# Kernel tuning notes

Hardware: AMD Instinct MI355X
Metric: run time of the kernel (lower is better)

Reference implementation:

```python
import jax, jax.numpy as jnp
import numpy as np

TOPK = 4
TEMP = 1.0
BN_EPS = 1e-5


def setup_inputs() -> dict:
    key = jax.random.key(0)
    ks = jax.random.split(key, 5)
    B, H, W = 8, 256, 256
    return {
        "img": jax.random.uniform(ks[0], (B, 3, H, W), dtype=jnp.float32),
        "feat": jax.random.normal(ks[1], (B, 64, H, W), dtype=jnp.float32),
        "w_bneck": jax.random.normal(ks[2], (16, 64), dtype=jnp.float32) * 0.1,
        "b_bneck": jax.random.normal(ks[3], (16,), dtype=jnp.float32) * 0.1,
        "gamma": jnp.ones((16,), dtype=jnp.float32),
        "beta": jnp.zeros((16,), dtype=jnp.float32),
        "w_mask": jax.random.normal(ks[4], (256, 16), dtype=jnp.float32) * 0.1,
        "num_colors": 64,
    }


def reference(img, feat, w_bneck, b_bneck, gamma, beta, w_mask, num_colors):
    B, _, H, W = img.shape
    # bottleneck: 1x1 conv + BatchNorm (training stats) + ReLU
    x = jnp.einsum('bchw,oc->bohw', feat, w_bneck) + b_bneck[None, :, None, None]
    mu = x.mean(axis=(0, 2, 3))
    var = x.var(axis=(0, 2, 3))
    x = (x - mu[None, :, None, None]) * jax.lax.rsqrt(var + BN_EPS)[None, :, None, None]
    x = jax.nn.relu(x * gamma[None, :, None, None] + beta[None, :, None, None])
    # color_mask: bias-free 1x1 conv -> [B, 256, H, W]
    m = jnp.einsum('bchw,oc->bohw', x, w_mask)
    # agg == 'mean': [B, 256//num_colors, num_colors, H, W].mean(1)
    m = m.reshape(B, -1, num_colors, H, W).mean(axis=1)  # [B, nc, H, W]
    # per-pixel topk over color channel + softmax + scatter mask
    k = min(TOPK, num_colors)
    m_l = jnp.transpose(m, (0, 2, 3, 1))          # [B, H, W, nc]
    vals, idx = jax.lax.top_k(m_l, k)             # [B, H, W, k]
    sm = jax.nn.softmax(vals / TEMP, axis=-1)
    bi = jnp.arange(B)[:, None, None, None]
    hi = jnp.arange(H)[None, :, None, None]
    wi = jnp.arange(W)[None, None, :, None]
    m_scat = jnp.zeros_like(m_l).at[bi, hi, wi, idx].set(sm)
    m = jnp.transpose(m_scat, (0, 3, 1, 2))       # [B, nc, H, W]
    # weighted color palette: [B, 3, nc, 1, 1]
    num = jnp.einsum('bchw,bnhw->bcn', img, m)
    den = m.sum(axis=(2, 3))                      # [B, nc]
    color_palette = (num / (den[:, None, :] + 1e-8))[:, :, :, None, None]
    # train-mode reconstruction
    transformed_img = jnp.einsum('bnhw,bcn->bchw', m, color_palette[:, :, :, 0, 0])
    return (transformed_img, m, color_palette)
```

## Files before the change

kernel.cpp:

```cpp
#include <hip/hip_runtime.h>

typedef long long ll;

#define PPI   65536
#define NPIX  524288
#define NCH   64
#define NB    16
#define NC    64
#define BN_EPS 1e-5

__global__ __launch_bounds__(256) void k_stats(const float* __restrict__ feat,
                                               const float* __restrict__ wb,
                                               const float* __restrict__ bb,
                                               double* __restrict__ gsum,
                                               double* __restrict__ gsq)
{
    const int P = 4;
    int tid = threadIdx.x;
    int b   = blockIdx.x >> 6;
    int p0  = (blockIdx.x & 63) * 1024 + tid;
    const float* fb = feat + (ll)b * NCH * PPI + p0;

    float acc[NB][P];
#pragma unroll
    for (int o = 0; o < NB; ++o)
#pragma unroll
        for (int j = 0; j < P; ++j) acc[o][j] = 0.f;

#pragma unroll 4
    for (int c = 0; c < NCH; ++c) {
        float f[P];
#pragma unroll
        for (int j = 0; j < P; ++j) f[j] = fb[(ll)c * PPI + j * 256];
#pragma unroll
        for (int o = 0; o < NB; ++o) {
            float wv = wb[o * NCH + c];
#pragma unroll
            for (int j = 0; j < P; ++j) acc[o][j] = fmaf(f[j], wv, acc[o][j]);
        }
    }

    __shared__ float wsum[4][NB];
    __shared__ float wsq[4][NB];
    int wave = tid >> 6, lane = tid & 63;
#pragma unroll
    for (int o = 0; o < NB; ++o) {
        float bo = bb[o];
        float s = 0.f, q = 0.f;
#pragma unroll
        for (int j = 0; j < P; ++j) { float x = acc[o][j] + bo; s += x; q = fmaf(x, x, q); }
        for (int off = 32; off > 0; off >>= 1) {
            s += __shfl_down(s, off);
            q += __shfl_down(q, off);
        }
        if (lane == 0) { wsum[wave][o] = s; wsq[wave][o] = q; }
    }
    __syncthreads();
    if (tid < NB) {
        double s = (double)wsum[0][tid] + wsum[1][tid] + wsum[2][tid] + wsum[3][tid];
        double q = (double)wsq[0][tid] + wsq[1][tid] + wsq[2][tid] + wsq[3][tid];
        atomicAdd(&gsum[tid], s);
        atomicAdd(&gsq[tid], q);
    }
}

__global__ void k_finalize(const double* __restrict__ gsum,
                           const double* __restrict__ gsq,
                           const float* __restrict__ gamma,
                           const float* __restrict__ beta,
                           const float* __restrict__ wm,
                           float* __restrict__ scl,
                           float* __restrict__ shf,
                           float* __restrict__ weff)
{
    int t = threadIdx.x;
    if (t < NB) {
        double mu  = gsum[t] / (double)NPIX;
        double var = gsq[t] / (double)NPIX - mu * mu;
        double sc  = (double)gamma[t] / sqrt(var + BN_EPS);
        scl[t] = (float)sc;
        shf[t] = (float)((double)beta[t] - mu * sc);
    }
    if (t < NC) {
#pragma unroll
        for (int o = 0; o < NB; ++o) {
            float v = 0.25f * (wm[(0 * 64 + t) * NB + o] + wm[(1 * 64 + t) * NB + o] +
                               wm[(2 * 64 + t) * NB + o] + wm[(3 * 64 + t) * NB + o]);
            weff[t * NB + o] = v;
        }
    }
}

__global__ __launch_bounds__(256) void k_main(const float* __restrict__ feat,
                                              const float* __restrict__ img,
                                              const float* __restrict__ wb,
                                              const float* __restrict__ bb,
                                              const float* __restrict__ scl,
                                              const float* __restrict__ shf,
                                              const float* __restrict__ weff,
                                              float* __restrict__ m_out,
                                              unsigned* __restrict__ idx_out,
                                              float* __restrict__ sm_out,
                                              float* __restrict__ den_g,
                                              float* __restrict__ num_g)
{
    const int P = 2;
    __shared__ float den_loc[NC];
    __shared__ float num_loc[3 * NC];
    int tid = threadIdx.x;
    if (tid < NC) den_loc[tid] = 0.f;
    if (tid < 3 * NC) num_loc[tid] = 0.f;
    __syncthreads();

    int b  = blockIdx.x >> 7;
    int p0 = (blockIdx.x & 127) * 512 + tid;
    const float* fb = feat + (ll)b * NCH * PPI + p0;

    float acc[NB][P];
#pragma unroll
    for (int o = 0; o < NB; ++o)
#pragma unroll
        for (int j = 0; j < P; ++j) acc[o][j] = 0.f;

#pragma unroll 4
    for (int c = 0; c < NCH; ++c) {
        float f[P];
#pragma unroll
        for (int j = 0; j < P; ++j) f[j] = fb[(ll)c * PPI + j * 256];
#pragma unroll
        for (int o = 0; o < NB; ++o) {
            float wv = wb[o * NCH + c];
#pragma unroll
            for (int j = 0; j < P; ++j) acc[o][j] = fmaf(f[j], wv, acc[o][j]);
        }
    }

#pragma unroll
    for (int o = 0; o < NB; ++o) {
        float sc = scl[o];
        float sh = fmaf(bb[o], sc, shf[o]);
#pragma unroll
        for (int j = 0; j < P; ++j) acc[o][j] = fmaxf(0.f, fmaf(acc[o][j], sc, sh));
    }

    float tv[P][4];
    int   ti[P][4];
#pragma unroll
    for (int j = 0; j < P; ++j)
#pragma unroll
        for (int k = 0; k < 4; ++k) { tv[j][k] = -3.4e38f; ti[j][k] = 0; }

    for (int n = 0; n < NC; ++n) {
        float v[P];
#pragma unroll
        for (int j = 0; j < P; ++j) v[j] = 0.f;
#pragma unroll
        for (int o = 0; o < NB; ++o) {
            float wv = weff[n * NB + o];
#pragma unroll
            for (int j = 0; j < P; ++j) v[j] = fmaf(acc[o][j], wv, v[j]);
        }
#pragma unroll
        for (int j = 0; j < P; ++j) {
            float vv = v[j];
            if (vv > tv[j][3]) {
                if (vv > tv[j][0]) {
                    tv[j][3] = tv[j][2]; ti[j][3] = ti[j][2];
                    tv[j][2] = tv[j][1]; ti[j][2] = ti[j][1];
                    tv[j][1] = tv[j][0]; ti[j][1] = ti[j][0];
                    tv[j][0] = vv;       ti[j][0] = n;
                } else if (vv > tv[j][1]) {
                    tv[j][3] = tv[j][2]; ti[j][3] = ti[j][2];
                    tv[j][2] = tv[j][1]; ti[j][2] = ti[j][1];
                    tv[j][1] = vv;       ti[j][1] = n;
                } else if (vv > tv[j][2]) {
                    tv[j][3] = tv[j][2]; ti[j][3] = ti[j][2];
                    tv[j][2] = vv;       ti[j][2] = n;
                } else {
                    tv[j][3] = vv;       ti[j][3] = n;
                }
            }
        }
    }

    float sm[P][4];
#pragma unroll
    for (int j = 0; j < P; ++j) {
        float m0 = tv[j][0];
        float e0 = 1.0f;
        float e1 = expf(tv[j][1] - m0);
        float e2 = expf(tv[j][2] - m0);
        float e3 = expf(tv[j][3] - m0);
        float Z  = e0 + e1 + e2 + e3;
        sm[j][0] = e0 / Z; sm[j][1] = e1 / Z; sm[j][2] = e2 / Z; sm[j][3] = e3 / Z;
    }

#pragma unroll 1
    for (int n = 0; n < NC; ++n) {
#pragma unroll
        for (int j = 0; j < P; ++j) {
            float val = 0.f;
            val = (n == ti[j][0]) ? sm[j][0] : val;
            val = (n == ti[j][1]) ? sm[j][1] : val;
            val = (n == ti[j][2]) ? sm[j][2] : val;
            val = (n == ti[j][3]) ? sm[j][3] : val;
            m_out[((ll)b * NC + n) * PPI + p0 + j * 256] = val;
        }
    }

#pragma unroll
    for (int j = 0; j < P; ++j) {
        int p = p0 + j * 256;
        ll gp = (ll)b * PPI + p;
        idx_out[gp] = (unsigned)ti[j][0] | ((unsigned)ti[j][1] << 8) |
                      ((unsigned)ti[j][2] << 16) | ((unsigned)ti[j][3] << 24);
        sm_out[gp]             = sm[j][0];
        sm_out[(ll)NPIX + gp]  = sm[j][1];
        sm_out[2ll * NPIX + gp] = sm[j][2];
        sm_out[3ll * NPIX + gp] = sm[j][3];
        float i0 = img[((ll)b * 3 + 0) * PPI + p];
        float i1 = img[((ll)b * 3 + 1) * PPI + p];
        float i2 = img[((ll)b * 3 + 2) * PPI + p];
#pragma unroll
        for (int k = 0; k < 4; ++k) {
            float s = sm[j][k];
            int   n = ti[j][k];
            atomicAdd(&den_loc[n], s);
            atomicAdd(&num_loc[n], s * i0);
            atomicAdd(&num_loc[NC + n], s * i1);
            atomicAdd(&num_loc[2 * NC + n], s * i2);
        }
    }
    __syncthreads();
    if (tid < NC)     atomicAdd(&den_g[b * NC + tid], den_loc[tid]);
    if (tid < 3 * NC) atomicAdd(&num_g[(ll)b * 3 * NC + tid], num_loc[tid]);
}

__global__ void k_palette(const float* __restrict__ den_g,
                          const float* __restrict__ num_g,
                          float* __restrict__ pal_out)
{
    int t = blockIdx.x * blockDim.x + threadIdx.x;
    if (t >= 8 * NC) return;
    int b = t >> 6, n = t & 63;
    float d = den_g[t] + 1e-8f;
#pragma unroll
    for (int c = 0; c < 3; ++c)
        pal_out[((ll)b * 3 + c) * NC + n] = num_g[((ll)b * 3 + c) * NC + n] / d;
}

__global__ __launch_bounds__(256) void k_recon(const unsigned* __restrict__ idx_in,
                                               const float* __restrict__ sm_in,
                                               const float* __restrict__ pal,
                                               float* __restrict__ tout)
{
    const int P = 4;
    __shared__ float lpal[3 * NC];
    int tid = threadIdx.x;
    int b   = blockIdx.x >> 6;
    int p0  = (blockIdx.x & 63) * 1024 + tid;
    if (tid < 3 * NC) lpal[tid] = pal[(ll)b * 3 * NC + tid];
    __syncthreads();

#pragma unroll
    for (int j = 0; j < P; ++j) {
        int p = p0 + j * 256;
        ll gp = (ll)b * PPI + p;
        unsigned pk = idx_in[gp];
        int t0 = pk & 255, t1 = (pk >> 8) & 255, t2 = (pk >> 16) & 255, t3 = pk >> 24;
        float s0 = sm_in[gp];
        float s1 = sm_in[(ll)NPIX + gp];
        float s2 = sm_in[2ll * NPIX + gp];
        float s3 = sm_in[3ll * NPIX + gp];
#pragma unroll
        for (int c = 0; c < 3; ++c) {
            float v = s0 * lpal[c * NC + t0] + s1 * lpal[c * NC + t1] +
                      s2 * lpal[c * NC + t2] + s3 * lpal[c * NC + t3];
            tout[((ll)b * 3 + c) * PPI + p] = v;
        }
    }
}

extern "C" void kernel_launch(void* const* d_in, const int* in_sizes, int n_in,
                              void* d_out, int out_size, void* d_ws, size_t ws_size,
                              hipStream_t stream)
{
    const float* img   = (const float*)d_in[0];
    const float* feat  = (const float*)d_in[1];
    const float* wb    = (const float*)d_in[2];
    const float* bb    = (const float*)d_in[3];
    const float* gamma = (const float*)d_in[4];
    const float* beta  = (const float*)d_in[5];
    const float* wm    = (const float*)d_in[6];

    char* ws = (char*)d_ws;
    double*   gsum  = (double*)(ws + 0);
    double*   gsq   = (double*)(ws + 128);
    float*    den_g = (float*)(ws + 256);
    float*    num_g = (float*)(ws + 2304);
    float*    weff  = (float*)(ws + 8448);
    float*    scl   = (float*)(ws + 12544);
    float*    shf   = (float*)(ws + 12608);
    unsigned* idx4  = (unsigned*)(ws + 12672);
    float*    smarr = (float*)(ws + 12672 + 4ll * NPIX);

    float* t_out   = (float*)d_out;
    float* m_out   = t_out + 3ll * NPIX;
    float* pal_out = m_out + 64ll * NPIX;

    hipMemsetAsync(ws, 0, 8448, stream);

    k_stats<<<NPIX / 1024, 256, 0, stream>>>(feat, wb, bb, gsum, gsq);
    k_finalize<<<1, 64, 0, stream>>>(gsum, gsq, gamma, beta, wm, scl, shf, weff);
    k_main<<<NPIX / 512, 256, 0, stream>>>(feat, img, wb, bb, scl, shf, weff,
                                           m_out, idx4, smarr, den_g, num_g);
    k_palette<<<2, 256, 0, stream>>>(den_g, num_g, pal_out);
    k_recon<<<NPIX / 1024, 256, 0, stream>>>(idx4, smarr, pal_out, t_out);
}
```

Before: 361.9 us.

## Store bottleneck conv output once, fold finalize/palette kernels, vectorize with float4

The feature 1x1 conv is now computed once. Its pre-BN output is stashed in the last 16 channel planes of the m output buffer, so the second full read of the 64-channel feature tensor goes away. BN finalize and weight averaging move into the mask kernel, and palette division moves into recon, cutting two launches. All kernels now process 4 contiguous pixels per thread with float4 loads and stores. Top-k becomes a branchless select network, and shared-memory atomics are split per wave. The scratch reuse of m_out relies on every mask block reading its stashed planes before any block overwrites them, and a block's own channel 48-63 writes to its own pixels happen after its read.

```diff
diff --git a/kernel.cpp b/kernel.cpp
--- a/kernel.cpp
+++ b/kernel.cpp
@@ -9,275 +9,254 @@
 #define NC    64
 #define BN_EPS 1e-5
 
-__global__ __launch_bounds__(256) void k_stats(const float* __restrict__ feat,
-                                               const float* __restrict__ wb,
-                                               const float* __restrict__ bb,
-                                               double* __restrict__ gsum,
-                                               double* __restrict__ gsq)
-{
-    const int P = 4;
-    int tid = threadIdx.x;
-    int b   = blockIdx.x >> 6;
-    int p0  = (blockIdx.x & 63) * 1024 + tid;
+__global__ __launch_bounds__(256) void k_conv(const float* __restrict__ feat,
+                                              const float* __restrict__ wb,
+                                              double* __restrict__ gsum,
+                                              double* __restrict__ gsq,
+                                              float* __restrict__ xout)
+{
+    const int tid = threadIdx.x;
+    const int wave = tid >> 6, lane = tid & 63;
+    const int b   = blockIdx.x >> 6;
+    const int p0  = ((blockIdx.x & 63) << 10) + (tid << 2);
     const float* fb = feat + (ll)b * NCH * PPI + p0;
 
-    float acc[NB][P];
-#pragma unroll
-    for (int o = 0; o < NB; ++o)
-#pragma unroll
-        for (int j = 0; j < P; ++j) acc[o][j] = 0.f;
+    float4 acc[NB];
+#pragma unroll
+    for (int o = 0; o < NB; ++o) acc[o] = make_float4(0.f, 0.f, 0.f, 0.f);
 
 #pragma unroll 4
     for (int c = 0; c < NCH; ++c) {
-        float f[P];
-#pragma unroll
-        for (int j = 0; j < P; ++j) f[j] = fb[(ll)c * PPI + j * 256];
+        float4 f = *reinterpret_cast<const float4*>(fb + (ll)c * PPI);
 #pragma unroll
         for (int o = 0; o < NB; ++o) {
             float wv = wb[o * NCH + c];
-#pragma unroll
-            for (int j = 0; j < P; ++j) acc[o][j] = fmaf(f[j], wv, acc[o][j]);
-        }
-    }
-
-    __shared__ float wsum[4][NB];
-    __shared__ float wsq[4][NB];
-    int wave = tid >> 6, lane = tid & 63;
+            acc[o].x = fmaf(f.x, wv, acc[o].x);
+            acc[o].y = fmaf(f.y, wv, acc[o].y);
+            acc[o].z = fmaf(f.z, wv, acc[o].z);
+            acc[o].w = fmaf(f.w, wv, acc[o].w);
+        }
+    }
+
+#pragma unroll
+    for (int o = 0; o < NB; ++o)
+        *reinterpret_cast<float4*>(xout + ((ll)(b * NC + 48 + o)) * PPI + p0) = acc[o];
+
+    __shared__ float red_s[4][NB], red_q[4][NB];
 #pragma unroll
     for (int o = 0; o < NB; ++o) {
-        float bo = bb[o];
-        float s = 0.f, q = 0.f;
-#pragma unroll
-        for (int j = 0; j < P; ++j) { float x = acc[o][j] + bo; s += x; q = fmaf(x, x, q); }
+        float s = (acc[o].x + acc[o].y) + (acc[o].z + acc[o].w);
+        float q = fmaf(acc[o].x, acc[o].x, acc[o].y * acc[o].y) +
+                  fmaf(acc[o].z, acc[o].z, acc[o].w * acc[o].w);
+#pragma unroll
         for (int off = 32; off > 0; off >>= 1) {
             s += __shfl_down(s, off);
             q += __shfl_down(q, off);
         }
-        if (lane == 0) { wsum[wave][o] = s; wsq[wave][o] = q; }
+        if (lane == 0) { red_s[wave][o] = s; red_q[wave][o] = q; }
     }
     __syncthreads();
     if (tid < NB) {
-        double s = (double)wsum[0][tid] + wsum[1][tid] + wsum[2][tid] + wsum[3][tid];
-        double q = (double)wsq[0][tid] + wsq[1][tid] + wsq[2][tid] + wsq[3][tid];
-        atomicAdd(&gsum[tid], s);
-        atomicAdd(&gsq[tid], q);
-    }
-}
-
-__global__ void k_finalize(const double* __restrict__ gsum,
-                           const double* __restrict__ gsq,
-                           const float* __restrict__ gamma,
-                           const float* __restrict__ beta,
-                           const float* __restrict__ wm,
-                           float* __restrict__ scl,
-                           float* __restrict__ shf,
-                           float* __restrict__ weff)
-{
-    int t = threadIdx.x;
-    if (t < NB) {
-        double mu  = gsum[t] / (double)NPIX;
-        double var = gsq[t] / (double)NPIX - mu * mu;
-        double sc  = (double)gamma[t] / sqrt(var + BN_EPS);
-        scl[t] = (float)sc;
-        shf[t] = (float)((double)beta[t] - mu * sc);
-    }
-    if (t < NC) {
+        atomicAdd(&gsum[tid], (double)red_s[0][tid] + red_s[1][tid] + red_s[2][tid] + red_s[3][tid]);
+        atomicAdd(&gsq[tid],  (double)red_q[0][tid] + red_q[1][tid] + red_q[2][tid] + red_q[3][tid]);
+    }
+}
+
+__global__ __launch_bounds__(256) void k_mask(const float* __restrict__ img,
+                                              const float* __restrict__ gamma,
+                                              const float* __restrict__ beta,
+                                              const float* __restrict__ wm,
+                                              const double* __restrict__ gsum,
+                                              const double* __restrict__ gsq,
+                                              float* __restrict__ den_g,
+                                              float* __restrict__ num_g,
+                                              float* m_out,
+                                              unsigned* __restrict__ idx_out,
+                                              float* __restrict__ sm_out)
+{
+    __shared__ float weff_l[NC][NB];
+    __shared__ float den_loc[4][NC];
+    __shared__ float num_loc[4][3 * NC];
+    __shared__ float scl_l[NB], shf_l[NB];
+
+    const int tid = threadIdx.x;
+    const int wave = tid >> 6;
+    const int b   = blockIdx.x >> 6;
+    const int p0  = ((blockIdx.x & 63) << 10) + (tid << 2);
+
+    for (int i = tid; i < NC * NB; i += 256) {
+        int n = i >> 4, o = i & 15;
+        weff_l[n][o] = 0.25f * (wm[n * NB + o] + wm[(64 + n) * NB + o] +
+                                wm[(128 + n) * NB + o] + wm[(192 + n) * NB + o]);
+    }
+    for (int i = tid; i < 4 * NC; i += 256) den_loc[i >> 6][i & 63] = 0.f;
+    for (int i = tid; i < 4 * 3 * NC; i += 256) num_loc[i / (3 * NC)][i % (3 * NC)] = 0.f;
+    if (tid < NB) {
+        double mu  = gsum[tid] * (1.0 / NPIX);
+        double var = gsq[tid] * (1.0 / NPIX) - mu * mu;
+        double sc  = (double)gamma[tid] / sqrt(var + BN_EPS);
+        scl_l[tid] = (float)sc;
+        shf_l[tid] = (float)((double)beta[tid] - mu * sc);
+    }
+    __syncthreads();
+
+    float4 xx[NB];
+#pragma unroll
+    for (int o = 0; o < NB; ++o)
+        xx[o] = *reinterpret_cast<const float4*>(m_out + ((ll)(b * NC + 48 + o)) * PPI + p0);
+#pragma unroll
+    for (int o = 0; o < NB; ++o) {
+        float sc = scl_l[o], sh = shf_l[o];
+        xx[o].x = fmaxf(0.f, fmaf(xx[o].x, sc, sh));
+        xx[o].y = fmaxf(0.f, fmaf(xx[o].y, sc, sh));
+        xx[o].z = fmaxf(0.f, fmaf(xx[o].z, sc, sh));
+        xx[o].w = fmaxf(0.f, fmaf(xx[o].w, sc, sh));
+    }
+
+    float tv[4][4];
+    int   ti[4][4];
+#pragma unroll
+    for (int j = 0; j < 4; ++j)
+#pragma unroll
+        for (int k = 0; k < 4; ++k) { tv[j][k] = -3.4e38f; ti[j][k] = 0; }
+
+#pragma unroll 2
+    for (int n = 0; n < NC; ++n) {
+        const float* wr = weff_l[n];
+        float4 v = make_float4(0.f, 0.f, 0.f, 0.f);
 #pragma unroll
         for (int o = 0; o < NB; ++o) {
-            float v = 0.25f * (wm[(0 * 64 + t) * NB + o] + wm[(1 * 64 + t) * NB + o] +
-                               wm[(2 * 64 + t) * NB + o] + wm[(3 * 64 + t) * NB + o]);
-            weff[t * NB + o] = v;
-        }
-    }
-}
-
-__global__ __launch_bounds__(256) void k_main(const float* __restrict__ feat,
-                                              const float* __restrict__ img,
-                                              const float* __restrict__ wb,
-                                              const float* __restrict__ bb,
-                                              const float* __restrict__ scl,
-                                              const float* __restrict__ shf,
-                                              const float* __restrict__ weff,
-                                              float* __restrict__ m_out,
-                                              unsigned* __restrict__ idx_out,
-                                              float* __restrict__ sm_out,
-                                              float* __restrict__ den_g,
-                                              float* __restrict__ num_g)
-{
-    const int P = 2;
-    __shared__ float den_loc[NC];
-    __shared__ float num_loc[3 * NC];
-    int tid = threadIdx.x;
-    if (tid < NC) den_loc[tid] = 0.f;
-    if (tid < 3 * NC) num_loc[tid] = 0.f;
-    __syncthreads();
-
-    int b  = blockIdx.x >> 7;
-    int p0 = (blockIdx.x & 127) * 512 + tid;
-    const float* fb = feat + (ll)b * NCH * PPI + p0;
-
-    float acc[NB][P];
-#pragma unroll
-    for (int o = 0; o < NB; ++o)
-#pragma unroll
-        for (int j = 0; j < P; ++j) acc[o][j] = 0.f;
-
-#pragma unroll 4
-    for (int c = 0; c < NCH; ++c) {
-        float f[P];
-#pragma unroll
-        for (int j = 0; j < P; ++j) f[j] = fb[(ll)c * PPI + j * 256];
-#pragma unroll
-        for (int o = 0; o < NB; ++o) {
-            float wv = wb[o * NCH + c];
-#pragma unroll
-            for (int j = 0; j < P; ++j) acc[o][j] = fmaf(f[j], wv, acc[o][j]);
-        }
-    }
-
-#pragma unroll
-    for (int o = 0; o < NB; ++o) {
-        float sc = scl[o];
-        float sh = fmaf(bb[o], sc, shf[o]);
-#pragma unroll
-        for (int j = 0; j < P; ++j) acc[o][j] = fmaxf(0.f, fmaf(acc[o][j], sc, sh));
-    }
-
-    float tv[P][4];
-    int   ti[P][4];
-#pragma unroll
-    for (int j = 0; j < P; ++j)
-#pragma unroll
-        for (int k = 0; k < 4; ++k) { tv[j][k] = -3.4e38f; ti[j][k] = 0; }
-
-    for (int n = 0; n < NC; ++n) {
-        float v[P];
-#pragma unroll
-        for (int j = 0; j < P; ++j) v[j] = 0.f;
-#pragma unroll
-        for (int o = 0; o < NB; ++o) {
-            float wv = weff[n * NB + o];
-#pragma unroll
-            for (int j = 0; j < P; ++j) v[j] = fmaf(acc[o][j], wv, v[j]);
-        }
-#pragma unroll
-        for (int j = 0; j < P; ++j) {
-            float vv = v[j];
-            if (vv > tv[j][3]) {
-                if (vv > tv[j][0]) {
-                    tv[j][3] = tv[j][2]; ti[j][3] = ti[j][2];
-                    tv[j][2] = tv[j][1]; ti[j][2] = ti[j][1];
-                    tv[j][1] = tv[j][0]; ti[j][1] = ti[j][0];
-                    tv[j][0] = vv;       ti[j][0] = n;
-                } else if (vv > tv[j][1]) {
-                    tv[j][3] = tv[j][2]; ti[j][3] = ti[j][2];
-                    tv[j][2] = tv[j][1]; ti[j][2] = ti[j][1];
-                    tv[j][1] = vv;       ti[j][1] = n;
-                } else if (vv > tv[j][2]) {
-                    tv[j][3] = tv[j][2]; ti[j][3] = ti[j][2];
-                    tv[j][2] = vv;       ti[j][2] = n;
-                } else {
-                    tv[j][3] = vv;       ti[j][3] = n;
-                }
-            }
-        }
-    }
-
-    float sm[P][4];
-#pragma unroll
-    for (int j = 0; j < P; ++j) {
-        float m0 = tv[j][0];
-        float e0 = 1.0f;
-        float e1 = expf(tv[j][1] - m0);
-        float e2 = expf(tv[j][2] - m0);
-        float e3 = expf(tv[j][3] - m0);
-        float Z  = e0 + e1 + e2 + e3;
-        sm[j][0] = e0 / Z; sm[j][1] = e1 / Z; sm[j][2] = e2 / Z; sm[j][3] = e3 / Z;
-    }
-
+            float w = wr[o];
+            v.x = fmaf(xx[o].x, w, v.x);
+            v.y = fmaf(xx[o].y, w, v.y);
+            v.z = fmaf(xx[o].z, w, v.z);
+            v.w = fmaf(xx[o].w, w, v.w);
+        }
+        float vv[4] = {v.x, v.y, v.z, v.w};
+#pragma unroll
+        for (int j = 0; j < 4; ++j) {
+            float x = vv[j];
+            bool c0 = x > tv[j][0];
+            bool c1 = x > tv[j][1];
+            bool c2 = x > tv[j][2];
+            bool c3 = x > tv[j][3];
+            tv[j][3] = c2 ? tv[j][2] : fmaxf(x, tv[j][3]);
+            ti[j][3] = c2 ? ti[j][2] : (c3 ? n : ti[j][3]);
+            tv[j][2] = c1 ? tv[j][1] : fmaxf(x, tv[j][2]);
+            ti[j][2] = c1 ? ti[j][1] : (c2 ? n : ti[j][2]);
+            tv[j][1] = c0 ? tv[j][0] : fmaxf(x, tv[j][1]);
+            ti[j][1] = c0 ? ti[j][0] : (c1 ? n : ti[j][1]);
+            tv[j][0] = fmaxf(x, tv[j][0]);
+            ti[j][0] = c0 ? n : ti[j][0];
+        }
+    }
+
+    float smx[4][4];
+#pragma unroll
+    for (int j = 0; j < 4; ++j) {
+        float e1 = expf(tv[j][1] - tv[j][0]);
+        float e2 = expf(tv[j][2] - tv[j][0]);
+        float e3 = expf(tv[j][3] - tv[j][0]);
+        float rz = 1.f / (1.f + e1 + e2 + e3);
+        smx[j][0] = rz; smx[j][1] = e1 * rz; smx[j][2] = e2 * rz; smx[j][3] = e3 * rz;
+    }
+
+#define SEL(j, n) (((ti[j][0] == (n)) ? smx[j][0] : 0.f) + \
+                   ((ti[j][1] == (n)) ? smx[j][1] : 0.f) + \
+                   ((ti[j][2] == (n)) ? smx[j][2] : 0.f) + \
+                   ((ti[j][3] == (n)) ? smx[j][3] : 0.f))
 #pragma unroll 1
     for (int n = 0; n < NC; ++n) {
-#pragma unroll
-        for (int j = 0; j < P; ++j) {
-            float val = 0.f;
-            val = (n == ti[j][0]) ? sm[j][0] : val;
-            val = (n == ti[j][1]) ? sm[j][1] : val;
-            val = (n == ti[j][2]) ? sm[j][2] : val;
-            val = (n == ti[j][3]) ? sm[j][3] : val;
-            m_out[((ll)b * NC + n) * PPI + p0 + j * 256] = val;
-        }
-    }
-
-#pragma unroll
-    for (int j = 0; j < P; ++j) {
-        int p = p0 + j * 256;
-        ll gp = (ll)b * PPI + p;
-        idx_out[gp] = (unsigned)ti[j][0] | ((unsigned)ti[j][1] << 8) |
-                      ((unsigned)ti[j][2] << 16) | ((unsigned)ti[j][3] << 24);
-        sm_out[gp]             = sm[j][0];
-        sm_out[(ll)NPIX + gp]  = sm[j][1];
-        sm_out[2ll * NPIX + gp] = sm[j][2];
-        sm_out[3ll * NPIX + gp] = sm[j][3];
-        float i0 = img[((ll)b * 3 + 0) * PPI + p];
-        float i1 = img[((ll)b * 3 + 1) * PPI + p];
-        float i2 = img[((ll)b * 3 + 2) * PPI + p];
+        float4 mv;
+        mv.x = SEL(0, n); mv.y = SEL(1, n); mv.z = SEL(2, n); mv.w = SEL(3, n);
+        *reinterpret_cast<float4*>(m_out + ((ll)(b * NC + n)) * PPI + p0) = mv;
+    }
+#undef SEL
+
+    ll gp = (ll)b * PPI + p0;
+    uint4 pk;
+    pk.x = (unsigned)ti[0][0] | ((unsigned)ti[0][1] << 8) | ((unsigned)ti[0][2] << 16) | ((unsigned)ti[0][3] << 24);
+    pk.y = (unsigned)ti[1][0] | ((unsigned)ti[1][1] << 8) | ((unsigned)ti[1][2] << 16) | ((unsigned)ti[1][3] << 24);
+    pk.z = (unsigned)ti[2][0] | ((unsigned)ti[2][1] << 8) | ((unsigned)ti[2][2] << 16) | ((unsigned)ti[2][3] << 24);
+    pk.w = (unsigned)ti[3][0] | ((unsigned)ti[3][1] << 8) | ((unsigned)ti[3][2] << 16) | ((unsigned)ti[3][3] << 24);
+    *reinterpret_cast<uint4*>(idx_out + gp) = pk;
+#pragma unroll
+    for (int k = 0; k < 4; ++k) {
+        float4 sv = make_float4(smx[0][k], smx[1][k], smx[2][k], smx[3][k]);
+        *reinterpret_cast<float4*>(sm_out + (ll)k * NPIX + gp) = sv;
+    }
+
+    float4 i0 = *reinterpret_cast<const float4*>(img + ((ll)b * 3 + 0) * PPI + p0);
+    float4 i1 = *reinterpret_cast<const float4*>(img + ((ll)b * 3 + 1) * PPI + p0);
+    float4 i2 = *reinterpret_cast<const float4*>(img + ((ll)b * 3 + 2) * PPI + p0);
+    float ir0[4] = {i0.x, i0.y, i0.z, i0.w};
+    float ir1[4] = {i1.x, i1.y, i1.z, i1.w};
+    float ir2[4] = {i2.x, i2.y, i2.z, i2.w};
+#pragma unroll
+    for (int j = 0; j < 4; ++j) {
 #pragma unroll
         for (int k = 0; k < 4; ++k) {
-            float s = sm[j][k];
+            float s = smx[j][k];
             int   n = ti[j][k];
-            atomicAdd(&den_loc[n], s);
-            atomicAdd(&num_loc[n], s * i0);
-            atomicAdd(&num_loc[NC + n], s * i1);
-            atomicAdd(&num_loc[2 * NC + n], s * i2);
-        }
-    }
-    __syncthreads();
-    if (tid < NC)     atomicAdd(&den_g[b * NC + tid], den_loc[tid]);
-    if (tid < 3 * NC) atomicAdd(&num_g[(ll)b * 3 * NC + tid], num_loc[tid]);
-}
-
-__global__ void k_palette(const float* __restrict__ den_g,
-                          const float* __restrict__ num_g,
-                          float* __restrict__ pal_out)
-{
-    int t = blockIdx.x * blockDim.x + threadIdx.x;
-    if (t >= 8 * NC) return;
-    int b = t >> 6, n = t & 63;
-    float d = den_g[t] + 1e-8f;
-#pragma unroll
-    for (int c = 0; c < 3; ++c)
-        pal_out[((ll)b * 3 + c) * NC + n] = num_g[((ll)b * 3 + c) * NC + n] / d;
+            atomicAdd(&den_loc[wave][n], s);
+            atomicAdd(&num_loc[wave][0 * NC + n], s * ir0[j]);
+            atomicAdd(&num_loc[wave][1 * NC + n], s * ir1[j]);
+            atomicAdd(&num_loc[wave][2 * NC + n], s * ir2[j]);
+        }
+    }
+    __syncthreads();
+    if (tid < NC)
+        atomicAdd(&den_g[b * NC + tid],
+                  den_loc[0][tid] + den_loc[1][tid] + den_loc[2][tid] + den_loc[3][tid]);
+    if (tid < 3 * NC)
+        atomicAdd(&num_g[(ll)b * 3 * NC + tid],
+                  num_loc[0][tid] + num_loc[1][tid] + num_loc[2][tid] + num_loc[3][tid]);
 }
 
 __global__ __launch_bounds__(256) void k_recon(const unsigned* __restrict__ idx_in,
                                                const float* __restrict__ sm_in,
-                                               const float* __restrict__ pal,
-                                               float* __restrict__ tout)
-{
-    const int P = 4;
-    __shared__ float lpal[3 * NC];
-    int tid = threadIdx.x;
-    int b   = blockIdx.x >> 6;
-    int p0  = (blockIdx.x & 63) * 1024 + tid;
-    if (tid < 3 * NC) lpal[tid] = pal[(ll)b * 3 * NC + tid];
-    __syncthreads();
-
-#pragma unroll
-    for (int j = 0; j < P; ++j) {
-        int p = p0 + j * 256;
-        ll gp = (ll)b * PPI + p;
-        unsigned pk = idx_in[gp];
-        int t0 = pk & 255, t1 = (pk >> 8) & 255, t2 = (pk >> 16) & 255, t3 = pk >> 24;
-        float s0 = sm_in[gp];
-        float s1 = sm_in[(ll)NPIX + gp];
-        float s2 = sm_in[2ll * NPIX + gp];
-        float s3 = sm_in[3ll * NPIX + gp];
-#pragma unroll
-        for (int c = 0; c < 3; ++c) {
-            float v = s0 * lpal[c * NC + t0] + s1 * lpal[c * NC + t1] +
-                      s2 * lpal[c * NC + t2] + s3 * lpal[c * NC + t3];
-            tout[((ll)b * 3 + c) * PPI + p] = v;
-        }
+                                               const float* __restrict__ den_g,
+                                               const float* __restrict__ num_g,
+                                               float* __restrict__ pal_out,
+                                               float* __restrict__ t_out)
+{
+    __shared__ float pal_l[3][NC];
+    __shared__ float rden[NC];
+    const int tid = threadIdx.x;
+    const int b   = blockIdx.x >> 6;
+    const int p0  = ((blockIdx.x & 63) << 10) + (tid << 2);
+
+    if (tid < NC) rden[tid] = 1.f / (den_g[b * NC + tid] + 1e-8f);
+    __syncthreads();
+    if (tid < 3 * NC) {
+        int c = tid >> 6, n = tid & 63;
+        pal_l[c][n] = num_g[(ll)b * 3 * NC + tid] * rden[n];
+    }
+    __syncthreads();
+    if ((blockIdx.x & 63) == 0 && tid < 3 * NC)
+        pal_out[b * 3 * NC + tid] = pal_l[tid >> 6][tid & 63];
+
+    ll gp = (ll)b * PPI + p0;
+    uint4 pk  = *reinterpret_cast<const uint4*>(idx_in + gp);
+    float4 s0 = *reinterpret_cast<const float4*>(sm_in + gp);
+    float4 s1 = *reinterpret_cast<const float4*>(sm_in + (ll)NPIX + gp);
+    float4 s2 = *reinterpret_cast<const float4*>(sm_in + 2ll * NPIX + gp);
+    float4 s3 = *reinterpret_cast<const float4*>(sm_in + 3ll * NPIX + gp);
+    unsigned pkv[4] = {pk.x, pk.y, pk.z, pk.w};
+    float sA[4][4] = {{s0.x, s1.x, s2.x, s3.x}, {s0.y, s1.y, s2.y, s3.y},
+                      {s0.z, s1.z, s2.z, s3.z}, {s0.w, s1.w, s2.w, s3.w}};
+
+#pragma unroll
+    for (int c = 0; c < 3; ++c) {
+        float4 t;
+        float* tp = &t.x;
+#pragma unroll
+        for (int j = 0; j < 4; ++j) {
+            unsigned p = pkv[j];
+            tp[j] = sA[j][0] * pal_l[c][p & 255] + sA[j][1] * pal_l[c][(p >> 8) & 255] +
+                    sA[j][2] * pal_l[c][(p >> 16) & 255] + sA[j][3] * pal_l[c][p >> 24];
+        }
+        *reinterpret_cast<float4*>(t_out + ((ll)b * 3 + c) * PPI + p0) = t;
     }
 }
 
@@ -288,7 +267,6 @@
     const float* img   = (const float*)d_in[0];
     const float* feat  = (const float*)d_in[1];
     const float* wb    = (const float*)d_in[2];
-    const float* bb    = (const float*)d_in[3];
     const float* gamma = (const float*)d_in[4];
     const float* beta  = (const float*)d_in[5];
     const float* wm    = (const float*)d_in[6];
@@ -298,11 +276,8 @@
     double*   gsq   = (double*)(ws + 128);
     float*    den_g = (float*)(ws + 256);
     float*    num_g = (float*)(ws + 2304);
-    float*    weff  = (float*)(ws + 8448);
-    float*    scl   = (float*)(ws + 12544);
-    float*    shf   = (float*)(ws + 12608);
-    unsigned* idx4  = (unsigned*)(ws + 12672);
-    float*    smarr = (float*)(ws + 12672 + 4ll * NPIX);
+    unsigned* idx4  = (unsigned*)(ws + 8448);
+    float*    smarr = (float*)(ws + 8448 + 4ll * NPIX);
 
     float* t_out   = (float*)d_out;
     float* m_out   = t_out + 3ll * NPIX;
@@ -310,10 +285,8 @@
 
     hipMemsetAsync(ws, 0, 8448, stream);
 
-    k_stats<<<NPIX / 1024, 256, 0, stream>>>(feat, wb, bb, gsum, gsq);
-    k_finalize<<<1, 64, 0, stream>>>(gsum, gsq, gamma, beta, wm, scl, shf, weff);
-    k_main<<<NPIX / 512, 256, 0, stream>>>(feat, img, wb, bb, scl, shf, weff,
-                                           m_out, idx4, smarr, den_g, num_g);
-    k_palette<<<2, 256, 0, stream>>>(den_g, num_g, pal_out);
-    k_recon<<<NPIX / 1024, 256, 0, stream>>>(idx4, smarr, pal_out, t_out);
-}
+    k_conv <<<NPIX / 1024, 256, 0, stream>>>(feat, wb, gsum, gsq, m_out);
+    k_mask <<<NPIX / 1024, 256, 0, stream>>>(img, gamma, beta, wm, gsum, gsq,
+                                             den_g, num_g, m_out, idx4, smarr);
+    k_recon<<<NPIX / 1024, 256, 0, stream>>>(idx4, smarr, den_g, num_g, pal_out, t_out);
+}
```

Measured after the change: 356.0 us. Within noise of the previous version (-1.7%).
